# Kernel optimization log

Measured on AMD Instinct MI355X. Metric: run time of the kernel, lower is better.

The kernel has to match this reference:

```python
import jax, jax.numpy as jnp
import numpy as np

B, S, D = 4, 2048, 1024
H = 8
HD = D // H            # 128 head dim
FF = 4096 // H         # 512 per-head expert hidden
E = 8                  # num experts
K = 2                  # top-k
MU, GAMMA = 0.7, 1.0
LN_EPS = 1e-5


def setup_inputs() -> dict:
    key = jax.random.key(0)
    ks = jax.random.split(key, 12)
    sc = lambda *shape: 1.0 / np.sqrt(shape[0])
    return {
        "x": jax.random.normal(ks[0], (B, S, D), jnp.float32),
        "momentum": jnp.zeros((B * S * H, HD), jnp.float32),
        # split proj (input_dim -> input_dim)
        "split_W": jax.random.normal(ks[1], (D, D), jnp.float32) * sc(D),
        "split_b": jnp.zeros((D,), jnp.float32),
        # gate (head_dim -> num_experts)
        "gate_W": jax.random.normal(ks[2], (HD, E), jnp.float32) * sc(HD),
        "gate_b": jnp.zeros((E,), jnp.float32),
        # stacked experts: Linear(HD->FF) ReLU Linear(FF->HD)
        "W1": jax.random.normal(ks[3], (E, HD, FF), jnp.float32) * sc(HD),
        "b1": jnp.zeros((E, FF), jnp.float32),
        "W2": jax.random.normal(ks[4], (E, FF, HD), jnp.float32) * sc(FF),
        "b2": jnp.zeros((E, HD), jnp.float32),
        # layernorm over head_dim
        "ln_g": jnp.ones((HD,), jnp.float32),
        "ln_b": jnp.zeros((HD,), jnp.float32),
        # merge proj
        "merge_W": jax.random.normal(ks[5], (D, D), jnp.float32) * sc(D),
        "merge_b": jnp.zeros((D,), jnp.float32),
    }


def _topk_gate(t, gate_W, gate_b):
    # t: [T, HD] -> dense gate weights [T, E] with only top-K nonzero
    logits = t @ gate_W + gate_b                       # [T, E]
    topv, topi = jax.lax.top_k(logits, K)              # [T, K]
    gates_k = jax.nn.softmax(topv, axis=-1)            # softmax over kept experts
    onehot = jax.nn.one_hot(topi, E, dtype=t.dtype)    # [T, K, E]
    return jnp.einsum("tk,tke->te", gates_k, onehot)   # scatter back


def reference(x, momentum, split_W, split_b, gate_W, gate_b,
              W1, b1, W2, b2, ln_g, ln_b, merge_W, merge_b):
    # split: [B,S,D] -> [B*S*H, HD]
    x_hat = x @ split_W + split_b
    t = x_hat.reshape(B * S * H, HD)

    gates = _topk_gate(t, gate_W, gate_b)              # [T, E]

    # all-experts dense compute (matches the source's per-expert loop)
    h = jax.nn.relu(jnp.einsum("td,edf->etf", t, W1) + b1[:, None, :])  # [E,T,FF]
    eo = jnp.einsum("etf,efd->etd", h, W2) + b2[:, None, :]             # [E,T,HD]
    expert_outputs = jnp.einsum("te,etd->td", gates, eo)                # [T,HD]

    new_momentum = -expert_outputs + MU * momentum
    out = t + GAMMA * new_momentum

    # layernorm over head_dim
    mean = out.mean(-1, keepdims=True)
    var = out.var(-1, keepdims=True)
    out = (out - mean) * jax.lax.rsqrt(var + LN_EPS) * ln_g + ln_b

    # merge: [T,HD] -> [B,S,D] -> linear
    o = out.reshape(B, S, D)
    final = o @ merge_W + merge_b
    return final, new_momentum
```

## Files before the change

kernel.cpp:

```cpp
#include <hip/hip_runtime.h>

#define NBATCH 4
#define NS 2048
#define ND 1024
#define NH 8
#define HD 128
#define NFF 512
#define NE 8
#define NT 65536
#define NBS 8192
#define MU_F 0.7f
#define LN_EPS_F 1e-5f

typedef __attribute__((ext_vector_type(4))) float f32x4;
typedef __attribute__((ext_vector_type(2))) double f64x2;
typedef __attribute__((ext_vector_type(8))) _Float16 f16x8;
typedef __attribute__((ext_vector_type(4))) _Float16 f16x4;
typedef __attribute__((ext_vector_type(2))) _Float16 f16x2;

__device__ __forceinline__ void gload_lds16(const void* g, void* l) {
  __builtin_amdgcn_global_load_lds(
      (const __attribute__((address_space(1))) unsigned int*)g,
      (__attribute__((address_space(3))) unsigned int*)l, 16, 0, 0);
}

__global__ void tr_cvt_kernel(const float* __restrict__ in, _Float16* __restrict__ out, int R, int C) {
  __shared__ float tile[32][33];
  int b = blockIdx.z;
  const float* inp = in + (size_t)b * R * C;
  _Float16* outp = out + (size_t)b * R * C;
  int c = blockIdx.x * 32 + threadIdx.x;
  int r0 = blockIdx.y * 32;
  #pragma unroll
  for (int i = 0; i < 4; i++) {
    int r = r0 + threadIdx.y + i * 8;
    tile[threadIdx.y + i * 8][threadIdx.x] = inp[(size_t)r * C + c];
  }
  __syncthreads();
  int rr = r0 + threadIdx.x;
  #pragma unroll
  for (int i = 0; i < 4; i++) {
    int cc = blockIdx.x * 32 + threadIdx.y + i * 8;
    outp[(size_t)cc * R + rr] = (_Float16)tile[threadIdx.x][threadIdx.y + i * 8];
  }
}

__global__ void build_G_kernel(const float* __restrict__ split_W, const float* __restrict__ split_b,
                               const float* __restrict__ gate_W, const float* __restrict__ gate_b,
                               double* __restrict__ G, double* __restrict__ gbias,
                               int* __restrict__ cnt) {
  int idx = blockIdx.x * 256 + threadIdx.x;
  if (blockIdx.x == 0 && threadIdx.x < 256) { cnt[threadIdx.x] = 0; cnt[threadIdx.x + 256] = 0; }
  int d = idx >> 6, o = idx & 63, h = o >> 3, e = o & 7;
  double acc = 0.0;
  const float* r0 = split_W + (size_t)d * ND + h * 128;
  #pragma unroll 4
  for (int j = 0; j < 128; j++)
    acc += (double)r0[j] * (double)gate_W[j * 8 + e];
  G[((size_t)(d >> 1) * 64 + o) * 2 + (d & 1)] = acc;
  if (idx < 64) {
    double bacc = 0.0;
    for (int j = 0; j < 128; j++)
      bacc += (double)split_b[h * 128 + j] * (double)gate_W[j * 8 + e];
    gbias[idx] = bacc + (double)gate_b[e];
  }
}

__global__ __launch_bounds__(256) void gate_kernel(const float* __restrict__ x,
    const f64x2* __restrict__ Gx2, const double* __restrict__ gbias,
    _Float16* __restrict__ x_h,
    float* __restrict__ tkw, int* __restrict__ lists, int* __restrict__ cnt) {
  __shared__ f64x2 Gs[32 * 64];
  __shared__ double xsd[16][66];
  __shared__ double lg[16 * 64];
  __shared__ int lcnt[8];
  __shared__ int lbase[8];
  int tid = threadIdx.x, lane = tid & 63, w = tid >> 6;
  int bs0 = blockIdx.x * 16;
  double acc[4];
  #pragma unroll
  for (int r = 0; r < 4; r++) acc[r] = 0.0;
  int xrow = tid >> 4, xc4 = tid & 15;
  const double* xr = &xsd[0][0] + (w * 4) * 66;
  if (tid < 8) lcnt[tid] = 0;

  for (int ch = 0; ch < 16; ch++) {
    __syncthreads();
    float4 xv4 = *(const float4*)(x + (size_t)(bs0 + xrow) * ND + ch * 64 + xc4 * 4);
    f64x2 xa = { (double)xv4.x, (double)xv4.y };
    f64x2 xb = { (double)xv4.z, (double)xv4.w };
    *(f64x2*)&xsd[xrow][xc4 * 4]     = xa;
    *(f64x2*)&xsd[xrow][xc4 * 4 + 2] = xb;
    f16x4 xh = { (_Float16)xv4.x, (_Float16)xv4.y, (_Float16)xv4.z, (_Float16)xv4.w };
    *(f16x4*)(x_h + (size_t)(bs0 + xrow) * ND + ch * 64 + xc4 * 4) = xh;
    #pragma unroll
    for (int j = 0; j < 8; j++) {
      int n = j * 256 + tid;
      gload_lds16(Gx2 + (size_t)ch * 2048 + n, Gs + n);
    }
    __syncthreads();
    #pragma unroll 4
    for (int kp = 0; kp < 32; kp++) {
      f64x2 g = Gs[kp * 64 + lane];
      #pragma unroll
      for (int r = 0; r < 4; r++) {
        f64x2 xv = *(const f64x2*)(xr + r * 66 + kp * 2);
        acc[r] += xv.x * g.x;
        acc[r] += xv.y * g.y;
      }
    }
  }
  double gb = gbias[lane];
  #pragma unroll
  for (int r = 0; r < 4; r++)
    lg[(w * 4 + r) * 64 + lane] = acc[r] + gb;
  __syncthreads();

  int i1 = 0, i2 = 0, token = 0, p1 = 0, p2 = 0;
  if (tid < 128) {
    int row = tid >> 3, h = tid & 7;
    const double* L = lg + row * 64 + h * 8;
    double v1 = L[0];
    #pragma unroll
    for (int e2 = 1; e2 < 8; e2++) if (L[e2] > v1) { v1 = L[e2]; i1 = e2; }
    i2 = -1; double v2 = -1e300;
    #pragma unroll
    for (int e2 = 0; e2 < 8; e2++) if (e2 != i1 && L[e2] > v2) { v2 = L[e2]; i2 = e2; }
    float ex = expf((float)(v2 - v1));
    float den = 1.f + ex;
    float g1 = 1.f / den, g2 = ex / den;
    token = (bs0 + row) * 8 + h;
    tkw[token * 2]     = g1;
    tkw[token * 2 + 1] = g2;
    p1 = atomicAdd(&lcnt[i1], 1);
    p2 = atomicAdd(&lcnt[i2], 1);
  }
  __syncthreads();
  if (tid < 8) lbase[tid] = atomicAdd(cnt + tid * 64, lcnt[tid]);
  __syncthreads();
  if (tid < 128) {
    lists[(size_t)i1 * NT + lbase[i1] + p1] = token * 2;
    lists[(size_t)i2 * NT + lbase[i2] + p2] = token * 2 + 1;
  }
}

__global__ __launch_bounds__(256) void gemm_f16_kernel(
    const _Float16* __restrict__ A, const _Float16* __restrict__ Bt,
    const float* __restrict__ bias, float* __restrict__ Cf, _Float16* __restrict__ Ch,
    int M, int N, int Kd) {
  __shared__ _Float16 As[128 * 32];
  __shared__ _Float16 Bs[128 * 32];
  int tid = threadIdx.x, lane = tid & 63, w = tid >> 6;
  int wr = w >> 1, wc = w & 1;
  int lid = blockIdx.y * 8 + blockIdx.x;
  int xcd = lid & 7, sub = (lid >> 3) & 7, grp = lid >> 6;
  int m0 = (xcd * 8 + sub) * 128;
  int n0 = grp * 128;
  f32x4 acc[4][4];
  #pragma unroll
  for (int i = 0; i < 4; i++)
    #pragma unroll
    for (int j = 0; j < 4; j++) acc[i][j] = (f32x4){0.f, 0.f, 0.f, 0.f};
  int srow = lane >> 2, scol = (lane & 3) * 8;
  int fr = lane & 15, ko = (lane >> 4) * 8;
  const _Float16* Ag = A + (size_t)(m0 + srow) * Kd + scol;
  const _Float16* Bg = Bt + (size_t)(n0 + srow) * Kd + scol;

  for (int k0 = 0; k0 < Kd; k0 += 32) {
    #pragma unroll
    for (int j = 0; j < 2; j++) {
      int rb = (w * 2 + j) * 16;
      gload_lds16(Ag + (size_t)rb * Kd + k0, As + rb * 32);
      gload_lds16(Bg + (size_t)rb * Kd + k0, Bs + rb * 32);
    }
    __syncthreads();
    f16x8 af[4], bq[4];
    #pragma unroll
    for (int mi = 0; mi < 4; mi++) af[mi] = *(const f16x8*)(As + (wr * 64 + mi * 16 + fr) * 32 + ko);
    #pragma unroll
    for (int ni = 0; ni < 4; ni++) bq[ni] = *(const f16x8*)(Bs + (wc * 64 + ni * 16 + fr) * 32 + ko);
    __syncthreads();
    #pragma unroll
    for (int mi = 0; mi < 4; mi++)
      #pragma unroll
      for (int ni = 0; ni < 4; ni++)
        acc[mi][ni] = __builtin_amdgcn_mfma_f32_16x16x32_f16(af[mi], bq[ni], acc[mi][ni], 0, 0, 0);
  }
  int rbase = m0 + wr * 64 + ((lane >> 4) << 2);
  int cbase = n0 + wc * 64 + (lane & 15);
  #pragma unroll
  for (int mi = 0; mi < 4; mi++)
    #pragma unroll
    for (int ni = 0; ni < 4; ni++) {
      int cc = cbase + ni * 16;
      float bv = bias ? bias[cc] : 0.f;
      #pragma unroll
      for (int r = 0; r < 4; r++) {
        int rr = rbase + mi * 16 + r;
        float v = acc[mi][ni][r] + bv;
        if (Cf) Cf[(size_t)rr * N + cc] = v;
        if (Ch) Ch[(size_t)rr * N + cc] = (_Float16)v;
      }
    }
}

__global__ __launch_bounds__(512, 2) void expert_kernel(
    const _Float16* __restrict__ t_h, const _Float16* __restrict__ W1t, const _Float16* __restrict__ W2t,
    const float* __restrict__ b1, const float* __restrict__ b2,
    const int* __restrict__ cnt, const int* __restrict__ lists, const float* __restrict__ tkw,
    _Float16* __restrict__ slots) {
  int e = blockIdx.x & 7;
  int m0 = (blockIdx.x >> 3) * 128;
  int count = cnt[e * 64];
  if (m0 >= count) return;
  __shared__ _Float16 ring[3][64 * 128];
  __shared__ _Float16 h_s[128 * 64];
  __shared__ float b1s[NFF];
  __shared__ float b2s[HD];
  __shared__ int alist[128];
  __shared__ float aw[128];
  int tid = threadIdx.x, lane = tid & 63, w = tid >> 6;
  int wr = w >> 1, wc = w & 1;
  int fr = lane & 15, g = lane >> 4;

  if (tid < 128) {
    int idx = m0 + tid;
    int a = (idx < count) ? lists[(size_t)e * NT + idx] : -1;
    alist[tid] = a;
    aw[tid] = (a >= 0) ? tkw[a] : 0.f;
  }
  b1s[tid] = b1[e * NFF + tid];
  if (tid < 128) b2s[tid] = b2[e * HD + tid];
  __syncthreads();

  auto stage = [&](int p) {
    if (p >= 16) return;
    int ch = p >> 1;
    _Float16* dst = &ring[p % 3][0];
    if ((p & 1) == 0) {
      #pragma unroll
      for (int j = 0; j < 2; j++) {
        int n = j * 512 + tid;
        int r = n >> 4, gg = n & 15;
        int sg = gg ^ ((r >> 1) & 7);
        gload_lds16(W1t + (size_t)e * (NFF * HD) + (size_t)(ch * 64 + r) * HD + sg * 8, dst + n * 8);
      }
    } else {
      #pragma unroll
      for (int j = 0; j < 2; j++) {
        int n = j * 512 + tid;
        int r = n >> 3, gg = n & 7;
        int sg = gg ^ ((r >> 1) & 7);
        gload_lds16(W2t + (size_t)e * (HD * NFF) + (size_t)r * NFF + ch * 64 + sg * 8, dst + n * 8);
      }
    }
  };

  f16x8 af[2][4];
  #pragma unroll
  for (int mi = 0; mi < 2; mi++) {
    int rloc = wr * 32 + mi * 16 + fr;
    int a = alist[rloc];
    const _Float16* tb = t_h + (size_t)(a >> 1) * HD;
    #pragma unroll
    for (int ks = 0; ks < 4; ks++) {
      f16x8 v = {0, 0, 0, 0, 0, 0, 0, 0};
      if (a >= 0) v = *(const f16x8*)(tb + ks * 32 + g * 8);
      af[mi][ks] = v;
    }
  }
  asm volatile("s_waitcnt vmcnt(0)" ::: "memory");
  stage(0); stage(1);
  asm volatile("s_waitcnt vmcnt(2) lgkmcnt(0)\n\ts_barrier" ::: "memory");

  f32x4 acc2[2][4];
  #pragma unroll
  for (int i = 0; i < 2; i++)
    #pragma unroll
    for (int j = 0; j < 4; j++) acc2[i][j] = (f32x4){0.f, 0.f, 0.f, 0.f};

  #pragma unroll
  for (int p = 0; p < 16; p++) {
    stage(p + 2);
    int ch = p >> 1;
    const char* WB = (const char*)&ring[p % 3][0];
    if ((p & 1) == 0) {
      float b1r[2][4];
      #pragma unroll
      for (int ni = 0; ni < 2; ni++)
        #pragma unroll
        for (int r = 0; r < 4; r++)
          b1r[ni][r] = b1s[ch * 64 + wc * 32 + ni * 16 + g * 4 + r];
      f32x4 acc1[2][2];
      #pragma unroll
      for (int i = 0; i < 2; i++)
        #pragma unroll
        for (int j = 0; j < 2; j++) acc1[i][j] = (f32x4){0.f, 0.f, 0.f, 0.f};
      #pragma unroll
      for (int ks = 0; ks < 4; ks++) {
        f16x8 bq[2];
        #pragma unroll
        for (int ni = 0; ni < 2; ni++) {
          int rw = wc * 32 + ni * 16 + fr;
          int byte = rw * 256 + ((ks * 64 + g * 16) ^ (((rw >> 1) & 7) << 4));
          bq[ni] = *(const f16x8*)(WB + byte);
        }
        #pragma unroll
        for (int mi = 0; mi < 2; mi++)
          #pragma unroll
          for (int ni = 0; ni < 2; ni++)
            acc1[mi][ni] = __builtin_amdgcn_mfma_f32_16x16x32_f16(bq[ni], af[mi][ks], acc1[mi][ni], 0, 0, 0);
      }
      #pragma unroll
      for (int mi = 0; mi < 2; mi++)
        #pragma unroll
        for (int ni = 0; ni < 2; ni++) {
          f16x4 hv;
          #pragma unroll
          for (int r = 0; r < 4; r++)
            hv[r] = (_Float16)fmaxf(acc1[mi][ni][r] + b1r[ni][r], 0.f);
          int tok = wr * 32 + mi * 16 + fr;
          int foff = wc * 64 + ni * 32 + g * 8;
          int byte = tok * 128 + (foff ^ (((tok >> 1) & 7) << 4));
          *(f16x4*)((char*)h_s + byte) = hv;
        }
    } else {
      #pragma unroll
      for (int ks = 0; ks < 2; ks++) {
        f16x8 ah[2], bq[4];
        #pragma unroll
        for (int mi = 0; mi < 2; mi++) {
          int row = wr * 32 + mi * 16 + fr;
          int byte = row * 128 + ((ks * 64 + g * 16) ^ (((row >> 1) & 7) << 4));
          ah[mi] = *(const f16x8*)((const char*)h_s + byte);
        }
        #pragma unroll
        for (int ni = 0; ni < 4; ni++) {
          int rw = wc * 64 + ni * 16 + fr;
          int byte = rw * 128 + ((ks * 64 + g * 16) ^ (((rw >> 1) & 7) << 4));
          bq[ni] = *(const f16x8*)((const char*)&ring[p % 3][0] + byte);
        }
        #pragma unroll
        for (int mi = 0; mi < 2; mi++)
          #pragma unroll
          for (int ni = 0; ni < 4; ni++)
            acc2[mi][ni] = __builtin_amdgcn_mfma_f32_16x16x32_f16(ah[mi], bq[ni], acc2[mi][ni], 0, 0, 0);
      }
    }
    if (p == 14) {
      asm volatile("s_waitcnt vmcnt(0) lgkmcnt(0)\n\ts_barrier" ::: "memory");
    } else if (p < 14) {
      asm volatile("s_waitcnt vmcnt(2) lgkmcnt(0)\n\ts_barrier" ::: "memory");
    }
  }
  #pragma unroll
  for (int mi = 0; mi < 2; mi++)
    #pragma unroll
    for (int ni = 0; ni < 4; ni++) {
      int ncol = wc * 64 + ni * 16 + fr;
      float bv = b2s[ncol];
      #pragma unroll
      for (int r = 0; r < 4; r++) {
        int m = wr * 32 + mi * 16 + g * 4 + r;
        int a = alist[m];
        if (a >= 0)
          slots[(size_t)a * HD + ncol] = (_Float16)(aw[m] * (acc2[mi][ni][r] + bv));
      }
    }
}

__global__ __launch_bounds__(256) void combine_ln_kernel(
    const _Float16* __restrict__ slots, const float* __restrict__ momentum,
    const _Float16* __restrict__ t_h, const float* __restrict__ ln_g, const float* __restrict__ ln_b,
    float* __restrict__ nm_out, _Float16* __restrict__ out_h) {
  int w = threadIdx.x >> 6, lane = threadIdx.x & 63;
  int tok = blockIdx.x * 4 + w;
  int d0 = lane * 2;
  f16x2 s0 = *(const f16x2*)(slots + (size_t)tok * 256 + d0);
  f16x2 s1 = *(const f16x2*)(slots + (size_t)tok * 256 + 128 + d0);
  float2 mo = *(const float2*)(momentum + (size_t)tok * HD + d0);
  f16x2 tv = *(const f16x2*)(t_h + (size_t)tok * HD + d0);
  float nm0 = -((float)s0.x + (float)s1.x) + MU_F * mo.x;
  float nm1 = -((float)s0.y + (float)s1.y) + MU_F * mo.y;
  float2 nm2; nm2.x = nm0; nm2.y = nm1;
  *(float2*)(nm_out + (size_t)tok * HD + d0) = nm2;
  float r0 = (float)tv.x + nm0;
  float r1 = (float)tv.y + nm1;
  float s = r0 + r1, sq = r0 * r0 + r1 * r1;
  #pragma unroll
  for (int m = 1; m < 64; m <<= 1) { s += __shfl_xor(s, m, 64); sq += __shfl_xor(sq, m, 64); }
  float mean = s * (1.f / 128.f);
  float var = sq * (1.f / 128.f) - mean * mean;
  float is = rsqrtf(var + LN_EPS_F);
  float y0 = (r0 - mean) * is * ln_g[d0] + ln_b[d0];
  float y1 = (r1 - mean) * is * ln_g[d0 + 1] + ln_b[d0 + 1];
  f16x2 yo = { (_Float16)y0, (_Float16)y1 };
  *(f16x2*)(out_h + (size_t)tok * HD + d0) = yo;
}

extern "C" void kernel_launch(void* const* d_in, const int* in_sizes, int n_in,
                              void* d_out, int out_size, void* d_ws, size_t ws_size,
                              hipStream_t stream) {
  const float* x        = (const float*)d_in[0];
  const float* momentum = (const float*)d_in[1];
  const float* split_W  = (const float*)d_in[2];
  const float* split_b  = (const float*)d_in[3];
  const float* gate_W   = (const float*)d_in[4];
  const float* gate_b   = (const float*)d_in[5];
  const float* W1       = (const float*)d_in[6];
  const float* b1       = (const float*)d_in[7];
  const float* W2       = (const float*)d_in[8];
  const float* b2       = (const float*)d_in[9];
  const float* ln_g     = (const float*)d_in[10];
  const float* ln_b     = (const float*)d_in[11];
  const float* merge_W  = (const float*)d_in[12];
  const float* merge_b  = (const float*)d_in[13];
  float* final_out = (float*)d_out;
  float* nm_out    = final_out + (size_t)NBS * ND;

  char* ws = (char*)d_ws;
  size_t off = 0;
  auto alloc = [&](size_t bytes) { void* p = ws + off; off = (off + bytes + 255) & ~(size_t)255; return p; };
  _Float16* x_h   = (_Float16*)alloc((size_t)NBS * ND * 2);
  _Float16* t_h   = (_Float16*)alloc((size_t)NT * HD * 2);
  _Float16* out_h = (_Float16*)alloc((size_t)NT * HD * 2);
  _Float16* sWt   = (_Float16*)alloc((size_t)ND * ND * 2);
  _Float16* mWt   = (_Float16*)alloc((size_t)ND * ND * 2);
  _Float16* W1t   = (_Float16*)alloc((size_t)NE * HD * NFF * 2);
  _Float16* W2t   = (_Float16*)alloc((size_t)NE * HD * NFF * 2);
  f64x2*    Gx2   = (f64x2*)alloc((size_t)512 * 64 * 16);
  double*   gbias = (double*)alloc(64 * 8);
  float*    tkw   = (float*)alloc((size_t)NT * 2 * 4);
  int*      lists = (int*)alloc((size_t)NE * NT * 4);
  int*      cnt   = (int*)alloc(512 * 4);
  _Float16* slots = (_Float16*)alloc((size_t)NT * 2 * HD * 2);
  (void)in_sizes; (void)n_in; (void)out_size; (void)ws_size;

  tr_cvt_kernel<<<dim3(32, 32, 1), dim3(32, 8), 0, stream>>>(split_W, sWt, ND, ND);
  tr_cvt_kernel<<<dim3(32, 32, 1), dim3(32, 8), 0, stream>>>(merge_W, mWt, ND, ND);
  tr_cvt_kernel<<<dim3(16, 4, 8), dim3(32, 8), 0, stream>>>(W1, W1t, HD, NFF);
  tr_cvt_kernel<<<dim3(4, 16, 8), dim3(32, 8), 0, stream>>>(W2, W2t, NFF, HD);
  build_G_kernel<<<256, 256, 0, stream>>>(split_W, split_b, gate_W, gate_b, (double*)Gx2, gbias, cnt);
  gate_kernel<<<512, 256, 0, stream>>>(x, Gx2, gbias, x_h, tkw, lists, cnt);
  gemm_f16_kernel<<<dim3(8, 64), 256, 0, stream>>>(x_h, sWt, split_b, nullptr, t_h, NBS, ND, ND);
  expert_kernel<<<NE * 512, 512, 0, stream>>>(t_h, W1t, W2t, b1, b2, cnt, lists, tkw, slots);
  combine_ln_kernel<<<NT / 4, 256, 0, stream>>>(slots, momentum, t_h, ln_g, ln_b, nm_out, out_h);
  gemm_f16_kernel<<<dim3(8, 64), 256, 0, stream>>>(out_h, mWt, merge_b, final_out, nullptr, NBS, ND, ND);
}
```

Measured before the change: 235.1 us.

## Compute gate logits in fp32 with fp64 fallback near ties; fuse transpose launches

The gate kernel now computes the folded gate logits in fp32 (reading x straight from global with wave-uniform addresses) instead of fp64 staged through LDS. When the top-1/top-2 or top-2/top-3 margins fall below a small epsilon, it recomputes that token's logits in fp64 so expert selection stays exact. This targets the slow fp64 FMA rate, at the cost of a divergent, serial fallback path whose cost depends on how often near-ties occur. The four weight transpose/convert launches are also merged into one kernel to cut launch overhead.

```diff
diff --git a/kernel.cpp b/kernel.cpp
--- a/kernel.cpp
+++ b/kernel.cpp
@@ -11,6 +11,7 @@
 #define NBS 8192
 #define MU_F 0.7f
 #define LN_EPS_F 1e-5f
+#define EPS_GATE 2e-3f
 
 typedef __attribute__((ext_vector_type(4))) float f32x4;
 typedef __attribute__((ext_vector_type(2))) double f64x2;
@@ -24,13 +25,21 @@
       (__attribute__((address_space(3))) unsigned int*)l, 16, 0, 0);
 }
 
-__global__ void tr_cvt_kernel(const float* __restrict__ in, _Float16* __restrict__ out, int R, int C) {
+__global__ void tr_cvt_all_kernel(const float* __restrict__ split_W, const float* __restrict__ merge_W,
+                                  const float* __restrict__ W1, const float* __restrict__ W2,
+                                  _Float16* __restrict__ sWt, _Float16* __restrict__ mWt,
+                                  _Float16* __restrict__ W1t, _Float16* __restrict__ W2t) {
   __shared__ float tile[32][33];
-  int b = blockIdx.z;
+  int id = blockIdx.x;
+  const float* in; _Float16* out; int R, C, bx, by, b;
+  if (id < 1024)      { in = split_W; out = sWt; R = ND;  C = ND;  bx = id & 31; by = id >> 5; b = 0; }
+  else if (id < 2048) { id -= 1024; in = merge_W; out = mWt; R = ND;  C = ND;  bx = id & 31; by = id >> 5; b = 0; }
+  else if (id < 2560) { id -= 2048; in = W1; out = W1t; R = HD;  C = NFF; bx = id & 15; by = (id >> 4) & 3; b = id >> 6; }
+  else                { id -= 2560; in = W2; out = W2t; R = NFF; C = HD;  bx = id & 3;  by = (id >> 2) & 15; b = id >> 6; }
   const float* inp = in + (size_t)b * R * C;
   _Float16* outp = out + (size_t)b * R * C;
-  int c = blockIdx.x * 32 + threadIdx.x;
-  int r0 = blockIdx.y * 32;
+  int c = bx * 32 + threadIdx.x;
+  int r0 = by * 32;
   #pragma unroll
   for (int i = 0; i < 4; i++) {
     int r = r0 + threadIdx.y + i * 8;
@@ -40,15 +49,15 @@
   int rr = r0 + threadIdx.x;
   #pragma unroll
   for (int i = 0; i < 4; i++) {
-    int cc = blockIdx.x * 32 + threadIdx.y + i * 8;
+    int cc = bx * 32 + threadIdx.y + i * 8;
     outp[(size_t)cc * R + rr] = (_Float16)tile[threadIdx.x][threadIdx.y + i * 8];
   }
 }
 
 __global__ void build_G_kernel(const float* __restrict__ split_W, const float* __restrict__ split_b,
                                const float* __restrict__ gate_W, const float* __restrict__ gate_b,
-                               double* __restrict__ G, double* __restrict__ gbias,
-                               int* __restrict__ cnt) {
+                               double* __restrict__ G, float* __restrict__ Gf,
+                               double* __restrict__ gbias, int* __restrict__ cnt) {
   int idx = blockIdx.x * 256 + threadIdx.x;
   if (blockIdx.x == 0 && threadIdx.x < 256) { cnt[threadIdx.x] = 0; cnt[threadIdx.x + 256] = 0; }
   int d = idx >> 6, o = idx & 63, h = o >> 3, e = o & 7;
@@ -57,7 +66,9 @@
   #pragma unroll 4
   for (int j = 0; j < 128; j++)
     acc += (double)r0[j] * (double)gate_W[j * 8 + e];
-  G[((size_t)(d >> 1) * 64 + o) * 2 + (d & 1)] = acc;
+  size_t pk = ((size_t)(d >> 1) * 64 + o) * 2 + (d & 1);
+  G[pk] = acc;
+  Gf[pk] = (float)acc;
   if (idx < 64) {
     double bacc = 0.0;
     for (int j = 0; j < 128; j++)
@@ -67,68 +78,94 @@
 }
 
 __global__ __launch_bounds__(256) void gate_kernel(const float* __restrict__ x,
-    const f64x2* __restrict__ Gx2, const double* __restrict__ gbias,
+    const float* __restrict__ Gf, const f64x2* __restrict__ Gx2, const double* __restrict__ gbias,
     _Float16* __restrict__ x_h,
     float* __restrict__ tkw, int* __restrict__ lists, int* __restrict__ cnt) {
-  __shared__ f64x2 Gs[32 * 64];
-  __shared__ double xsd[16][66];
-  __shared__ double lg[16 * 64];
+  __shared__ float Gsf[32 * 128];
+  __shared__ float lg[16 * 64];
   __shared__ int lcnt[8];
   __shared__ int lbase[8];
   int tid = threadIdx.x, lane = tid & 63, w = tid >> 6;
   int bs0 = blockIdx.x * 16;
-  double acc[4];
-  #pragma unroll
-  for (int r = 0; r < 4; r++) acc[r] = 0.0;
+  float accA[4], accB[4];
+  #pragma unroll
+  for (int r = 0; r < 4; r++) { accA[r] = 0.f; accB[r] = 0.f; }
   int xrow = tid >> 4, xc4 = tid & 15;
-  const double* xr = &xsd[0][0] + (w * 4) * 66;
+  int rb = __builtin_amdgcn_readfirstlane(bs0 + w * 4);
   if (tid < 8) lcnt[tid] = 0;
 
   for (int ch = 0; ch < 16; ch++) {
     __syncthreads();
     float4 xv4 = *(const float4*)(x + (size_t)(bs0 + xrow) * ND + ch * 64 + xc4 * 4);
-    f64x2 xa = { (double)xv4.x, (double)xv4.y };
-    f64x2 xb = { (double)xv4.z, (double)xv4.w };
-    *(f64x2*)&xsd[xrow][xc4 * 4]     = xa;
-    *(f64x2*)&xsd[xrow][xc4 * 4 + 2] = xb;
     f16x4 xh = { (_Float16)xv4.x, (_Float16)xv4.y, (_Float16)xv4.z, (_Float16)xv4.w };
     *(f16x4*)(x_h + (size_t)(bs0 + xrow) * ND + ch * 64 + xc4 * 4) = xh;
     #pragma unroll
-    for (int j = 0; j < 8; j++) {
+    for (int j = 0; j < 4; j++) {
       int n = j * 256 + tid;
-      gload_lds16(Gx2 + (size_t)ch * 2048 + n, Gs + n);
+      gload_lds16(Gf + (size_t)ch * 4096 + n * 4, Gsf + n * 4);
     }
     __syncthreads();
-    #pragma unroll 4
+    const float* xw = x + (size_t)rb * ND + ch * 64;
+    #pragma unroll 8
     for (int kp = 0; kp < 32; kp++) {
-      f64x2 g = Gs[kp * 64 + lane];
+      float2 g = *(const float2*)&Gsf[kp * 128 + lane * 2];
       #pragma unroll
       for (int r = 0; r < 4; r++) {
-        f64x2 xv = *(const f64x2*)(xr + r * 66 + kp * 2);
-        acc[r] += xv.x * g.x;
-        acc[r] += xv.y * g.y;
-      }
-    }
-  }
-  double gb = gbias[lane];
+        float xa = xw[r * ND + kp * 2];
+        float xb = xw[r * ND + kp * 2 + 1];
+        accA[r] = fmaf(xa, g.x, accA[r]);
+        accB[r] = fmaf(xb, g.y, accB[r]);
+      }
+    }
+  }
+  float gbf = (float)gbias[lane];
   #pragma unroll
   for (int r = 0; r < 4; r++)
-    lg[(w * 4 + r) * 64 + lane] = acc[r] + gb;
+    lg[(w * 4 + r) * 64 + lane] = accA[r] + accB[r] + gbf;
   __syncthreads();
 
   int i1 = 0, i2 = 0, token = 0, p1 = 0, p2 = 0;
   if (tid < 128) {
     int row = tid >> 3, h = tid & 7;
-    const double* L = lg + row * 64 + h * 8;
-    double v1 = L[0];
+    const float* L = lg + row * 64 + h * 8;
+    float v1 = L[0];
     #pragma unroll
     for (int e2 = 1; e2 < 8; e2++) if (L[e2] > v1) { v1 = L[e2]; i1 = e2; }
-    i2 = -1; double v2 = -1e300;
+    i2 = -1; float v2 = -1e30f;
     #pragma unroll
     for (int e2 = 0; e2 < 8; e2++) if (e2 != i1 && L[e2] > v2) { v2 = L[e2]; i2 = e2; }
-    float ex = expf((float)(v2 - v1));
-    float den = 1.f + ex;
-    float g1 = 1.f / den, g2 = ex / den;
+    float v3 = -1e30f;
+    #pragma unroll
+    for (int e2 = 0; e2 < 8; e2++) if (e2 != i1 && e2 != i2 && L[e2] > v3) v3 = L[e2];
+    float g1, g2;
+    if ((v1 - v2 >= EPS_GATE) && (v2 - v3 >= EPS_GATE)) {
+      float ex = expf(v2 - v1);
+      float den = 1.f + ex;
+      g1 = 1.f / den; g2 = ex / den;
+    } else {
+      double L64[8];
+      #pragma unroll
+      for (int e2 = 0; e2 < 8; e2++) L64[e2] = gbias[h * 8 + e2];
+      const float* xr = x + (size_t)(bs0 + row) * ND;
+      for (int kp = 0; kp < 512; kp++) {
+        double x0 = (double)xr[kp * 2], x1 = (double)xr[kp * 2 + 1];
+        const f64x2* gp = Gx2 + (size_t)kp * 64 + h * 8;
+        #pragma unroll
+        for (int e2 = 0; e2 < 8; e2++) {
+          f64x2 g = gp[e2];
+          L64[e2] += x0 * g.x + x1 * g.y;
+        }
+      }
+      i1 = 0; double d1 = L64[0];
+      #pragma unroll
+      for (int e2 = 1; e2 < 8; e2++) if (L64[e2] > d1) { d1 = L64[e2]; i1 = e2; }
+      i2 = -1; double d2 = -1e300;
+      #pragma unroll
+      for (int e2 = 0; e2 < 8; e2++) if (e2 != i1 && L64[e2] > d2) { d2 = L64[e2]; i2 = e2; }
+      float ex = expf((float)(d2 - d1));
+      float den = 1.f + ex;
+      g1 = 1.f / den; g2 = ex / den;
+    }
     token = (bs0 + row) * 8 + h;
     tkw[token * 2]     = g1;
     tkw[token * 2 + 1] = g2;
@@ -429,6 +466,7 @@
   _Float16* W1t   = (_Float16*)alloc((size_t)NE * HD * NFF * 2);
   _Float16* W2t   = (_Float16*)alloc((size_t)NE * HD * NFF * 2);
   f64x2*    Gx2   = (f64x2*)alloc((size_t)512 * 64 * 16);
+  float*    Gf    = (float*)alloc((size_t)512 * 64 * 8);
   double*   gbias = (double*)alloc(64 * 8);
   float*    tkw   = (float*)alloc((size_t)NT * 2 * 4);
   int*      lists = (int*)alloc((size_t)NE * NT * 4);
@@ -436,12 +474,9 @@
   _Float16* slots = (_Float16*)alloc((size_t)NT * 2 * HD * 2);
   (void)in_sizes; (void)n_in; (void)out_size; (void)ws_size;
 
-  tr_cvt_kernel<<<dim3(32, 32, 1), dim3(32, 8), 0, stream>>>(split_W, sWt, ND, ND);
-  tr_cvt_kernel<<<dim3(32, 32, 1), dim3(32, 8), 0, stream>>>(merge_W, mWt, ND, ND);
-  tr_cvt_kernel<<<dim3(16, 4, 8), dim3(32, 8), 0, stream>>>(W1, W1t, HD, NFF);
-  tr_cvt_kernel<<<dim3(4, 16, 8), dim3(32, 8), 0, stream>>>(W2, W2t, NFF, HD);
-  build_G_kernel<<<256, 256, 0, stream>>>(split_W, split_b, gate_W, gate_b, (double*)Gx2, gbias, cnt);
-  gate_kernel<<<512, 256, 0, stream>>>(x, Gx2, gbias, x_h, tkw, lists, cnt);
+  tr_cvt_all_kernel<<<3072, dim3(32, 8), 0, stream>>>(split_W, merge_W, W1, W2, sWt, mWt, W1t, W2t);
+  build_G_kernel<<<256, 256, 0, stream>>>(split_W, split_b, gate_W, gate_b, (double*)Gx2, Gf, gbias, cnt);
+  gate_kernel<<<512, 256, 0, stream>>>(x, Gf, Gx2, gbias, x_h, tkw, lists, cnt);
   gemm_f16_kernel<<<dim3(8, 64), 256, 0, stream>>>(x_h, sWt, split_b, nullptr, t_h, NBS, ND, ND);
   expert_kernel<<<NE * 512, 512, 0, stream>>>(t_h, W1t, W2t, b1, b2, cnt, lists, tkw, slots);
   combine_ln_kernel<<<NT / 4, 256, 0, stream>>>(slots, momentum, t_h, ln_g, ln_b, nm_out, out_h);
```

Result: slower. 351.0 us (+49.3%).
